# Kernel tuning notes

Measured on AMD Instinct MI355X. Metric: run time of the kernel, lower is better.

The kernel has to match this reference:

```python
import jax, jax.numpy as jnp
import numpy as np

SMOOTHING = 0.1
EPSILON = 1e-08


def setup_inputs() -> dict:
    key = jax.random.key(0)
    k1, k2 = jax.random.split(key)
    B, S, C = 2, 2048, 32000
    outputs = jax.random.normal(k1, (B, S, C), dtype=jnp.float32)
    gold_label_ids = jax.random.randint(k2, (B, S), 0, C, dtype=jnp.int64)
    mask = jnp.ones((B, S), dtype=bool)
    weight = jnp.ones((C,), dtype=jnp.float32)
    return {"outputs": outputs, "gold_label_ids": gold_label_ids, "mask": mask, "weight": weight}


def reference(outputs, gold_label_ids, mask, weight):
    B, S, C = outputs.shape
    N = B * S
    logits = outputs.reshape(N, C)
    gold = gold_label_ids.reshape(N)

    nll = -jax.nn.log_softmax(logits, axis=-1)  # [N, C]

    # Label-smoothed target: uniform = s/(C-1) everywhere, confidence at gold.
    # loss_i = sum_c w_c * nll_ic * smooth_ic
    #        = uniform * sum_c(w_c * nll_ic) + (confidence - uniform) * w_g * nll_ig
    uniform = SMOOTHING / (C - 1)
    confidence = 1.0 - SMOOTHING
    total = jnp.einsum('nc,c->n', nll, weight)  # sum of weighted nll per row
    gold_nll = jnp.take_along_axis(nll, gold[:, None], axis=1)[:, 0]
    gold_w = weight[gold]
    loss = uniform * total + (confidence - uniform) * gold_w * gold_nll  # [N]

    seq_mask = mask.reshape(N).astype(loss.dtype)
    loss = loss * seq_mask
    return jnp.sum(loss) / (jnp.sum(seq_mask) + EPSILON)
```

## Files before the change

kernel.cpp:

```cpp
#include <hip/hip_runtime.h>
#include <math.h>

#define SMOOTHING 0.1f
#define EPSILON_F 1e-8f

__device__ __forceinline__ void osm_combine(float& m, float& s, float mo, float so) {
    float nm = fmaxf(m, mo);
    s = s * __expf(m - nm) + so * __expf(mo - nm);
    m = nm;
}

__global__ __launch_bounds__(256) void Seq2SeqLoss_row_kernel(
    const float* __restrict__ logits,
    const int*   __restrict__ gold,
    const int*   __restrict__ mask,
    const float* __restrict__ weight,
    float*       __restrict__ row_loss,
    int C)
{
    const int row = blockIdx.x;
    const int tid = threadIdx.x;
    const float* __restrict__ x = logits + (size_t)row * (size_t)C;

    const int C4 = C >> 2;
    const float4* __restrict__ x4 = (const float4*)x;
    const float4* __restrict__ w4 = (const float4*)weight;

    float m0 = -1e30f, m1 = -1e30f, m2 = -1e30f, m3 = -1e30f;
    float s0 = 0.f, s1 = 0.f, s2 = 0.f, s3 = 0.f;
    float wd = 0.f, wsum = 0.f;

    for (int i = tid; i < C4; i += 256) {
        float4 v = x4[i];
        float4 w = w4[i];

        {
            float d = v.x - m0; float e = __expf(-fabsf(d)); bool gt = d > 0.f;
            s0 = fmaf(s0, gt ? e : 1.0f, gt ? 1.0f : e); m0 = fmaxf(m0, v.x);
        }
        {
            float d = v.y - m1; float e = __expf(-fabsf(d)); bool gt = d > 0.f;
            s1 = fmaf(s1, gt ? e : 1.0f, gt ? 1.0f : e); m1 = fmaxf(m1, v.y);
        }
        {
            float d = v.z - m2; float e = __expf(-fabsf(d)); bool gt = d > 0.f;
            s2 = fmaf(s2, gt ? e : 1.0f, gt ? 1.0f : e); m2 = fmaxf(m2, v.z);
        }
        {
            float d = v.w - m3; float e = __expf(-fabsf(d)); bool gt = d > 0.f;
            s3 = fmaf(s3, gt ? e : 1.0f, gt ? 1.0f : e); m3 = fmaxf(m3, v.w);
        }

        wd = fmaf(w.x, v.x, wd); wd = fmaf(w.y, v.y, wd);
        wd = fmaf(w.z, v.z, wd); wd = fmaf(w.w, v.w, wd);
        wsum += (w.x + w.y) + (w.z + w.w);
    }

    osm_combine(m0, s0, m1, s1);
    osm_combine(m2, s2, m3, s3);
    osm_combine(m0, s0, m2, s2);
    float M = m0, S = s0;

    #pragma unroll
    for (int off = 32; off >= 1; off >>= 1) {
        float Mo = __shfl_down(M, off);
        float So = __shfl_down(S, off);
        wd   += __shfl_down(wd, off);
        wsum += __shfl_down(wsum, off);
        osm_combine(M, S, Mo, So);
    }

    __shared__ float shM[4], shS[4], shWD[4], shWS[4];
    const int wave = tid >> 6;
    if ((tid & 63) == 0) { shM[wave] = M; shS[wave] = S; shWD[wave] = wd; shWS[wave] = wsum; }
    __syncthreads();

    if (tid == 0) {
        #pragma unroll
        for (int w = 1; w < 4; ++w) {
            osm_combine(M, S, shM[w], shS[w]);
            wd   += shWD[w];
            wsum += shWS[w];
        }
        float logZ = M + logf(S);

        int   g  = gold[row];
        float xg = x[g];
        float wg = weight[g];

        const float uniform    = SMOOTHING / (float)(C - 1);
        const float confidence = 1.0f - SMOOTHING;

        float total    = logZ * wsum - wd;
        float gold_nll = logZ - xg;
        float loss = uniform * total + (confidence - uniform) * wg * gold_nll;

        loss *= (mask[row] != 0) ? 1.0f : 0.0f;
        row_loss[row] = loss;
    }
}

__global__ __launch_bounds__(256) void Seq2SeqLoss_finalize_kernel(
    const float* __restrict__ row_loss,
    const int*   __restrict__ mask,
    float*       __restrict__ out,
    int N)
{
    const int tid = threadIdx.x;
    float acc = 0.f, cnt = 0.f;
    for (int i = tid; i < N; i += 256) {
        acc += row_loss[i];
        cnt += (mask[i] != 0) ? 1.0f : 0.0f;
    }
    #pragma unroll
    for (int off = 32; off >= 1; off >>= 1) {
        acc += __shfl_down(acc, off);
        cnt += __shfl_down(cnt, off);
    }
    __shared__ float shA[4], shC[4];
    const int wave = tid >> 6;
    if ((tid & 63) == 0) { shA[wave] = acc; shC[wave] = cnt; }
    __syncthreads();
    if (tid == 0) {
        #pragma unroll
        for (int w = 1; w < 4; ++w) { acc += shA[w]; cnt += shC[w]; }
        out[0] = acc / (cnt + EPSILON_F);
    }
}

extern "C" void kernel_launch(void* const* d_in, const int* in_sizes, int n_in,
                              void* d_out, int out_size, void* d_ws, size_t ws_size,
                              hipStream_t stream) {
    const float* logits = (const float*)d_in[0];
    const int*   gold   = (const int*)d_in[1];
    const int*   mask   = (const int*)d_in[2];
    const float* weight = (const float*)d_in[3];

    const int N = in_sizes[1];
    const int C = in_sizes[3];

    float* row_loss = (float*)d_ws;

    Seq2SeqLoss_row_kernel<<<N, 256, 0, stream>>>(logits, gold, mask, weight, row_loss, C);
    Seq2SeqLoss_finalize_kernel<<<1, 256, 0, stream>>>(row_loss, mask, (float*)d_out, N);
}
```

Baseline: 675.4 us.

## Process four rows per block and use per-float4 online softmax update

Each block now handles four rows, loading the weight vector once and reusing it across the rows, and issuing four independent row loads per iteration. The online softmax update changes from per-element lanes to a per-float4 chunk max followed by five exps. Blocks drop from 4096 to 1024, which cuts per-block reduction overhead but leaves fewer blocks to spread over the CUs and raises register pressure.

Result: no change. 679.9 us (+0.7%).

```diff
diff --git a/kernel.cpp b/kernel.cpp
--- a/kernel.cpp
+++ b/kernel.cpp
@@ -3,11 +3,26 @@
 
 #define SMOOTHING 0.1f
 #define EPSILON_F 1e-8f
+#define ROWS_PER_BLOCK 4
 
 __device__ __forceinline__ void osm_combine(float& m, float& s, float mo, float so) {
     float nm = fmaxf(m, mo);
     s = s * __expf(m - nm) + so * __expf(mo - nm);
     m = nm;
+}
+
+__device__ __forceinline__ void osm_upd4(float& m, float& s, float& wd,
+                                         float4 v, float4 w) {
+    float cm = fmaxf(fmaxf(v.x, v.y), fmaxf(v.z, v.w));
+    float nm = fmaxf(m, cm);
+    float e  = __expf(m - nm);
+    float e0 = __expf(v.x - nm);
+    float e1 = __expf(v.y - nm);
+    float e2 = __expf(v.z - nm);
+    float e3 = __expf(v.w - nm);
+    s = fmaf(s, e, (e0 + e1) + (e2 + e3));
+    m = nm;
+    wd = fmaf(w.x, v.x, fmaf(w.y, v.y, fmaf(w.z, v.z, fmaf(w.w, v.w, wd))));
 }
 
 __global__ __launch_bounds__(256) void Seq2SeqLoss_row_kernel(
@@ -16,87 +31,89 @@
     const int*   __restrict__ mask,
     const float* __restrict__ weight,
     float*       __restrict__ row_loss,
-    int C)
+    int C, int N)
 {
-    const int row = blockIdx.x;
+    const int r0  = blockIdx.x * ROWS_PER_BLOCK;
     const int tid = threadIdx.x;
-    const float* __restrict__ x = logits + (size_t)row * (size_t)C;
+    const int C4  = C >> 2;
 
-    const int C4 = C >> 2;
-    const float4* __restrict__ x4 = (const float4*)x;
+    const float4* __restrict__ x0 = (const float4*)(logits + (size_t)min(r0 + 0, N - 1) * (size_t)C);
+    const float4* __restrict__ x1 = (const float4*)(logits + (size_t)min(r0 + 1, N - 1) * (size_t)C);
+    const float4* __restrict__ x2 = (const float4*)(logits + (size_t)min(r0 + 2, N - 1) * (size_t)C);
+    const float4* __restrict__ x3 = (const float4*)(logits + (size_t)min(r0 + 3, N - 1) * (size_t)C);
     const float4* __restrict__ w4 = (const float4*)weight;
 
-    float m0 = -1e30f, m1 = -1e30f, m2 = -1e30f, m3 = -1e30f;
-    float s0 = 0.f, s1 = 0.f, s2 = 0.f, s3 = 0.f;
-    float wd = 0.f, wsum = 0.f;
+    float m[ROWS_PER_BLOCK], s[ROWS_PER_BLOCK], wd[ROWS_PER_BLOCK];
+    #pragma unroll
+    for (int j = 0; j < ROWS_PER_BLOCK; ++j) { m[j] = -1e30f; s[j] = 0.f; wd[j] = 0.f; }
+    float wsum = 0.f;
 
     for (int i = tid; i < C4; i += 256) {
-        float4 v = x4[i];
-        float4 w = w4[i];
-
-        {
-            float d = v.x - m0; float e = __expf(-fabsf(d)); bool gt = d > 0.f;
-            s0 = fmaf(s0, gt ? e : 1.0f, gt ? 1.0f : e); m0 = fmaxf(m0, v.x);
-        }
-        {
-            float d = v.y - m1; float e = __expf(-fabsf(d)); bool gt = d > 0.f;
-            s1 = fmaf(s1, gt ? e : 1.0f, gt ? 1.0f : e); m1 = fmaxf(m1, v.y);
-        }
-        {
-            float d = v.z - m2; float e = __expf(-fabsf(d)); bool gt = d > 0.f;
-            s2 = fmaf(s2, gt ? e : 1.0f, gt ? 1.0f : e); m2 = fmaxf(m2, v.z);
-        }
-        {
-            float d = v.w - m3; float e = __expf(-fabsf(d)); bool gt = d > 0.f;
-            s3 = fmaf(s3, gt ? e : 1.0f, gt ? 1.0f : e); m3 = fmaxf(m3, v.w);
-        }
-
-        wd = fmaf(w.x, v.x, wd); wd = fmaf(w.y, v.y, wd);
-        wd = fmaf(w.z, v.z, wd); wd = fmaf(w.w, v.w, wd);
+        float4 w  = w4[i];
+        float4 v0 = x0[i];
+        float4 v1 = x1[i];
+        float4 v2 = x2[i];
+        float4 v3 = x3[i];
         wsum += (w.x + w.y) + (w.z + w.w);
+        osm_upd4(m[0], s[0], wd[0], v0, w);
+        osm_upd4(m[1], s[1], wd[1], v1, w);
+        osm_upd4(m[2], s[2], wd[2], v2, w);
+        osm_upd4(m[3], s[3], wd[3], v3, w);
     }
-
-    osm_combine(m0, s0, m1, s1);
-    osm_combine(m2, s2, m3, s3);
-    osm_combine(m0, s0, m2, s2);
-    float M = m0, S = s0;
 
     #pragma unroll
     for (int off = 32; off >= 1; off >>= 1) {
-        float Mo = __shfl_down(M, off);
-        float So = __shfl_down(S, off);
-        wd   += __shfl_down(wd, off);
         wsum += __shfl_down(wsum, off);
-        osm_combine(M, S, Mo, So);
+        #pragma unroll
+        for (int j = 0; j < ROWS_PER_BLOCK; ++j) {
+            float Mo = __shfl_down(m[j], off);
+            float So = __shfl_down(s[j], off);
+            wd[j]   += __shfl_down(wd[j], off);
+            osm_combine(m[j], s[j], Mo, So);
+        }
     }
 
-    __shared__ float shM[4], shS[4], shWD[4], shWS[4];
+    __shared__ float shM[4][ROWS_PER_BLOCK], shS[4][ROWS_PER_BLOCK],
+                     shWD[4][ROWS_PER_BLOCK], shWS[4];
     const int wave = tid >> 6;
-    if ((tid & 63) == 0) { shM[wave] = M; shS[wave] = S; shWD[wave] = wd; shWS[wave] = wsum; }
+    if ((tid & 63) == 0) {
+        #pragma unroll
+        for (int j = 0; j < ROWS_PER_BLOCK; ++j) {
+            shM[wave][j] = m[j]; shS[wave][j] = s[j]; shWD[wave][j] = wd[j];
+        }
+        shWS[wave] = wsum;
+    }
     __syncthreads();
 
     if (tid == 0) {
         #pragma unroll
         for (int w = 1; w < 4; ++w) {
-            osm_combine(M, S, shM[w], shS[w]);
-            wd   += shWD[w];
             wsum += shWS[w];
+            #pragma unroll
+            for (int j = 0; j < ROWS_PER_BLOCK; ++j) {
+                osm_combine(m[j], s[j], shM[w][j], shS[w][j]);
+                wd[j] += shWD[w][j];
+            }
         }
-        float logZ = M + logf(S);
-
-        int   g  = gold[row];
-        float xg = x[g];
-        float wg = weight[g];
 
         const float uniform    = SMOOTHING / (float)(C - 1);
         const float confidence = 1.0f - SMOOTHING;
 
-        float total    = logZ * wsum - wd;
-        float gold_nll = logZ - xg;
-        float loss = uniform * total + (confidence - uniform) * wg * gold_nll;
-
-        loss *= (mask[row] != 0) ? 1.0f : 0.0f;
-        row_loss[row] = loss;
+        #pragma unroll
+        for (int j = 0; j < ROWS_PER_BLOCK; ++j) {
+            int row = r0 + j;
+            if (row < N) {
+                float logZ = m[j] + logf(s[j]);
+                int   g  = gold[row];
+                float xg = logits[(size_t)row * (size_t)C + g];
+                float wg = weight[g];
+                float total    = logZ * wsum - wd[j];
+                float gold_nll = logZ - xg;
+                float loss = uniform * total + (confidence - uniform) * wg * gold_nll;
+                loss *= (mask[row] != 0) ? 1.0f : 0.0f;
+                row_loss[row] = loss;
+            }
+        }
     }
 }
 
@@ -141,6 +158,8 @@
 
     float* row_loss = (float*)d_ws;
 
-    Seq2SeqLoss_row_kernel<<<N, 256, 0, stream>>>(logits, gold, mask, weight, row_loss, C);
+    const int nblocks = (N + ROWS_PER_BLOCK - 1) / ROWS_PER_BLOCK;
+    Seq2SeqLoss_row_kernel<<<nblocks, 256, 0, stream>>>(logits, gold, mask, weight,
+                                                        row_loss, C, N);
     Seq2SeqLoss_finalize_kernel<<<1, 256, 0, stream>>>(row_loss, mask, (float*)d_out, N);
 }
```
